# Kernel optimization log

Measured on AMD Instinct MI355X. Metric: run time of the kernel, lower is better.

Reference implementation:

```python
import math
import jax, jax.numpy as jnp
import numpy as np

R, N, B, E, H, M = 128, 256, 1, 512, 8, 4
D = E // H
NEG = -1e9  # eye-mask fill value from masked_fill(-1000000000)


def setup_inputs() -> dict:
    key = jax.random.key(0)
    ks = jax.random.split(key, 10)
    p = lambda k, shape: jax.random.normal(k, shape, jnp.float32) * 0.02
    z = lambda n: jnp.zeros((n,), jnp.float32)
    return {
        "x": jax.random.normal(ks[0], (R, N, B, E), jnp.float32),
        "network": jax.random.uniform(ks[1], (B, N, N, M), jnp.float32),
        "Wq": p(ks[2], (E, E)), "bq": z(E),
        "Wk": p(ks[3], (E, E)), "bk": z(E),
        "Wv": p(ks[4], (E, E)), "bv": z(E),
        "Wo": p(ks[5], (E, E)), "bo": z(E),
        "Wq1": p(ks[6], (D, 8)), "bq1": z(8),
        "Wk1": p(ks[7], (1, 8)), "bk1": z(8),
        "l": jax.random.normal(ks[8], (H, 1, 1, 1), jnp.float32),
    }


def reference(x, network, Wq, bq, Wk, bk, Wv, bv, Wo, bo, Wq1, bq1, Wk1, bk1, l):
    # x: [R, N, B, E]; network: [B, N, N, M] (B must be 1, as in the torch module)
    scaling = (D ** -0.5) / math.sqrt(R)  # align_scaling

    q = (x @ Wq + bq).reshape(R, N, B, H, D) * scaling
    k = (x @ Wk + bk).reshape(R, N, B, H, D)

    # shared contraction: summed over rows r, kept per head-dim d -> [H, B, N, N, D]
    qk = jnp.einsum('rinhd,rjnhd->hnijd', q, k)

    # network-bias MLP branch
    q1 = (qk @ Wq1 + bq1).mean(0)                  # [B, N, N, 8]
    network_k = network[..., None] * Wk1[0] + bk1  # Linear(1,8): [B, N, N, M, 8]
    net_attn = jnp.einsum('nijd,nijmd->nijm', q1, network_k)  # [B, N, N, M]
    net_attn = jnp.tile(net_attn, (H, 1, 1, 1))    # repeat over heads (B==1) -> [H, N, N, M]

    # attn_weights 'rinhd,rjnhd->hnij' == qk summed over d
    attn_weights = qk.sum(-1)                      # [H, B, N, N]

    net_probs = jax.nn.softmax(net_attn, axis=-1)  # softmax over M network channels
    net_bias = (network * net_probs).sum(-1)[:, None, :, :]  # [H, 1(B), N, N]
    attn_weights = attn_weights + l * net_bias

    eye = jnp.eye(N, dtype=bool)
    attn_weights = jnp.where(eye, NEG, attn_weights)
    attn_probs = jax.nn.softmax(attn_weights, axis=-1)  # [H, B, N, N]

    v = (x @ Wv + bv).reshape(R, N, B, H, D)
    context = jnp.einsum('hnij,rjnhd->rinhd', attn_probs, v).reshape(R, N, B, E)
    output = context @ Wo + bo
    return (output, attn_probs, l)
```

## Files before the change

kernel.cpp:

```cpp
#include <hip/hip_runtime.h>
#include <hip/hip_bf16.h>
#include <cmath>
#include <stdint.h>

using bf16 = __hip_bfloat16;
typedef __attribute__((ext_vector_type(8))) short bf16x8;
typedef __attribute__((ext_vector_type(4))) float f32x4;

constexpr int LDT  = 40;
constexpr int LDTB = 34;

__device__ __forceinline__ void gload16(const bf16* g, bf16* l)
{
  __builtin_amdgcn_global_load_lds(
      (const __attribute__((address_space(1))) void*)g,
      (__attribute__((address_space(3))) void*)l,
      16, 0, 0);
}

__global__ __launch_bounds__(256)
void k_convert_x(const float* __restrict__ x, bf16* __restrict__ xb)
{
  const long idx = (long)blockIdx.x * 256 + threadIdx.x;
  const float4 f0 = *(const float4*)&x[idx * 8];
  const float4 f1 = *(const float4*)&x[idx * 8 + 4];
  alignas(16) bf16 t[8] = {
    __float2bfloat16(f0.x), __float2bfloat16(f0.y),
    __float2bfloat16(f0.z), __float2bfloat16(f0.w),
    __float2bfloat16(f1.x), __float2bfloat16(f1.y),
    __float2bfloat16(f1.z), __float2bfloat16(f1.w)};
  *(uint4*)&xb[idx * 8] = *(const uint4*)t;
}

__global__ __launch_bounds__(256)
void k_prep_w(const float* __restrict__ Wq, const float* __restrict__ Wk,
              const float* __restrict__ Wv, const float* __restrict__ Wo,
              bf16* __restrict__ WT, float scaling)
{
  const int sel = blockIdx.z;
  const float* W = sel == 0 ? Wq : sel == 1 ? Wk : sel == 2 ? Wv : Wo;
  const float sc = sel == 0 ? scaling : 1.0f;
  const int k0 = blockIdx.x * 64, n0 = blockIdx.y * 64;
  __shared__ float tile[64][68];
  const int tid = threadIdx.x;
  #pragma unroll
  for (int it = 0; it < 4; it++) {
    const int c = tid + it * 256;
    const int kk = c >> 4, nn4 = (c & 15) * 4;
    const float4 v = *(const float4*)&W[(long)(k0 + kk) * 512 + n0 + nn4];
    tile[kk][nn4] = v.x; tile[kk][nn4 + 1] = v.y;
    tile[kk][nn4 + 2] = v.z; tile[kk][nn4 + 3] = v.w;
  }
  __syncthreads();
  #pragma unroll
  for (int it = 0; it < 2; it++) {
    const int c = tid + it * 256;
    const int nn = c >> 3, k8 = (c & 7) * 8;
    alignas(16) bf16 t[8];
    #pragma unroll
    for (int jj = 0; jj < 8; jj++) t[jj] = __float2bfloat16(tile[k8 + jj][nn] * sc);
    *(uint4*)&WT[(long)(sel * 512 + n0 + nn) * 512 + k0 + k8] = *(const uint4*)t;
  }
}

__global__ void k_prep_small(const float* __restrict__ bq, const float* __restrict__ bk,
                             const float* __restrict__ bv, const float* __restrict__ bo,
                             const float* __restrict__ Wq1, const float* __restrict__ Wk1,
                             float* __restrict__ bias_all, float* __restrict__ u, float scaling)
{
  const int idx = blockIdx.x * 256 + threadIdx.x;
  const int s2 = idx >> 9, n2 = idx & 511;
  const float* b = s2 == 0 ? bq : s2 == 1 ? bk : s2 == 2 ? bv : bo;
  bias_all[idx] = b[n2] * (s2 == 0 ? scaling : 1.0f);
  if (idx < 64) {
    float s = 0.0f;
    #pragma unroll
    for (int c = 0; c < 8; c++) s += Wq1[idx * 8 + c] * Wk1[c];
    u[idx] = s;
  }
}

__global__ __launch_bounds__(256)
void gemm_qkv(const bf16* __restrict__ xb, const bf16* __restrict__ WT,
              const float* __restrict__ bias_all,
              bf16* __restrict__ Qn, bf16* __restrict__ Kn, bf16* __restrict__ Vn)
{
  __shared__ bf16 As[2][128 * 32];
  __shared__ bf16 Bs[2][128 * 32];
  const int tid = threadIdx.x, lane = tid & 63;
  const int wid = tid >> 6, wr = wid >> 1, wc = wid & 1;
  const int lr = lane & 15, lk = (lane >> 4) * 8;
  const int flat = (blockIdx.x & 7) * 384 + (blockIdx.x >> 3);
  const int m0 = (flat / 12) * 128, n0 = (flat % 12) * 128;
  const int c1 = tid + 256;
  const int ra0 = tid >> 2, pa0 = (tid & 3) * 8;
  const int ra1 = c1 >> 2,  pa1 = (c1 & 3) * 8;
  f32x4 acc[4][4] = {};

  auto stage = [&](int b, int k0) {
    gload16(&xb[(long)(m0 + ra0) * 512 + k0 + pa0], &As[b][tid * 8]);
    gload16(&xb[(long)(m0 + ra1) * 512 + k0 + pa1], &As[b][c1 * 8]);
    gload16(&WT[(long)(n0 + ra0) * 512 + k0 + pa0], &Bs[b][tid * 8]);
    gload16(&WT[(long)(n0 + ra1) * 512 + k0 + pa1], &Bs[b][c1 * 8]);
  };

  stage(0, 0);
  asm volatile("s_waitcnt vmcnt(0)" ::: "memory");
  __syncthreads();

  int buf = 0;
  for (int t = 0; t < 16; ++t) {
    if (t < 15) stage(buf ^ 1, (t + 1) * 32);
    bf16x8 af[4], bfr[4];
    #pragma unroll
    for (int m = 0; m < 4; m++)
      af[m] = *(const bf16x8*)&As[buf][(wr * 64 + m * 16 + lr) * 32 + lk];
    #pragma unroll
    for (int n = 0; n < 4; n++)
      bfr[n] = *(const bf16x8*)&Bs[buf][(wc * 64 + n * 16 + lr) * 32 + lk];
    #pragma unroll
    for (int m = 0; m < 4; m++)
      #pragma unroll
      for (int n = 0; n < 4; n++)
        acc[m][n] = __builtin_amdgcn_mfma_f32_16x16x32_bf16(af[m], bfr[n], acc[m][n], 0, 0, 0);
    asm volatile("s_waitcnt vmcnt(0)" ::: "memory");
    __syncthreads();
    buf ^= 1;
  }

  const int er = (lane >> 4) * 4, ec = lane & 15;
  #pragma unroll
  for (int m = 0; m < 4; m++) {
    const int row0 = m0 + wr * 64 + m * 16 + er;
    #pragma unroll
    for (int n = 0; n < 4; n++) {
      const int col = n0 + wc * 64 + n * 16 + ec;
      const float bv = bias_all[col];
      #pragma unroll
      for (int q = 0; q < 4; q++) {
        const float v = acc[m][n][q] + bv;
        const long row = row0 + q;
        if (col < 512)       Qn[row * 512 + col]        = __float2bfloat16(v);
        else if (col < 1024) Kn[row * 512 + col - 512]  = __float2bfloat16(v);
        else                 Vn[row * 512 + col - 1024] = __float2bfloat16(v);
      }
    }
  }
}

__global__ __launch_bounds__(256)
void gemm_logits(const bf16* __restrict__ Qn, const bf16* __restrict__ Kn,
                 const float* __restrict__ u, float* __restrict__ part)
{
  __shared__ bf16 As[2][128 * 32];
  __shared__ bf16 Bs[2][128 * 32];
  __shared__ float us[64];
  const int tid = threadIdx.x, lane = tid & 63;
  const int wid = tid >> 6, wr = wid >> 1, wc = wid & 1;
  const int lr = lane & 15, lk = (lane >> 4) * 8;
  const int z = blockIdx.z, batch = z >> 3, ks = z & 7, h = batch & 7;
  const bool uscale = batch >= 8;
  const int m0 = blockIdx.y * 128, n0 = blockIdx.x * 128;
  if (tid < 64) us[tid] = u[tid];
  __syncthreads();
  const int c1 = tid + 256;
  const int ra0 = tid >> 2, pa0 = (tid & 3) * 8;
  const int ra1 = c1 >> 2,  pa1 = (c1 & 3) * 8;
  f32x4 acc[4][4] = {};

  auto gk_of = [&](int kk) { return ks * 1024 + kk * 32; };

  {
    const int gk = gk_of(0), r = gk >> 6, d0 = gk & 63;
    const long ab = (long)(r * 256 + m0) * 512 + h * 64 + d0;
    const long bb = (long)(r * 256 + n0) * 512 + h * 64 + d0;
    gload16(&Kn[bb + (long)ra0 * 512 + pa0], &Bs[0][tid * 8]);
    gload16(&Kn[bb + (long)ra1 * 512 + pa1], &Bs[0][c1 * 8]);
    if (!uscale) {
      gload16(&Qn[ab + (long)ra0 * 512 + pa0], &As[0][tid * 8]);
      gload16(&Qn[ab + (long)ra1 * 512 + pa1], &As[0][c1 * 8]);
    } else {
      const uint4 v0 = *(const uint4*)&Qn[ab + (long)ra0 * 512 + pa0];
      const uint4 v1 = *(const uint4*)&Qn[ab + (long)ra1 * 512 + pa1];
      const unsigned short* p0 = (const unsigned short*)&v0;
      const unsigned short* p1 = (const unsigned short*)&v1;
      alignas(16) bf16 t0[8], t1[8];
      #pragma unroll
      for (int jj = 0; jj < 8; jj++) {
        t0[jj] = __float2bfloat16(__bfloat162float(*(const bf16*)&p0[jj]) * us[d0 + pa0 + jj]);
        t1[jj] = __float2bfloat16(__bfloat162float(*(const bf16*)&p1[jj]) * us[d0 + pa1 + jj]);
      }
      *(uint4*)&As[0][tid * 8] = *(const uint4*)t0;
      *(uint4*)&As[0][c1 * 8] = *(const uint4*)t1;
    }
  }
  __syncthreads();

  int buf = 0;
  for (int kk = 0; kk < 32; ++kk) {
    uint4 va0, va1;
    int d0n = 0;
    if (kk < 31) {
      const int gk = gk_of(kk + 1), r = gk >> 6;
      d0n = gk & 63;
      const long ab = (long)(r * 256 + m0) * 512 + h * 64 + d0n;
      const long bb = (long)(r * 256 + n0) * 512 + h * 64 + d0n;
      gload16(&Kn[bb + (long)ra0 * 512 + pa0], &Bs[buf ^ 1][tid * 8]);
      gload16(&Kn[bb + (long)ra1 * 512 + pa1], &Bs[buf ^ 1][c1 * 8]);
      if (!uscale) {
        gload16(&Qn[ab + (long)ra0 * 512 + pa0], &As[buf ^ 1][tid * 8]);
        gload16(&Qn[ab + (long)ra1 * 512 + pa1], &As[buf ^ 1][c1 * 8]);
      } else {
        va0 = *(const uint4*)&Qn[ab + (long)ra0 * 512 + pa0];
        va1 = *(const uint4*)&Qn[ab + (long)ra1 * 512 + pa1];
      }
    }
    bf16x8 af[4], bfr[4];
    #pragma unroll
    for (int m = 0; m < 4; m++)
      af[m] = *(const bf16x8*)&As[buf][(wr * 64 + m * 16 + lr) * 32 + lk];
    #pragma unroll
    for (int n = 0; n < 4; n++)
      bfr[n] = *(const bf16x8*)&Bs[buf][(wc * 64 + n * 16 + lr) * 32 + lk];
    #pragma unroll
    for (int m = 0; m < 4; m++)
      #pragma unroll
      for (int n = 0; n < 4; n++)
        acc[m][n] = __builtin_amdgcn_mfma_f32_16x16x32_bf16(af[m], bfr[n], acc[m][n], 0, 0, 0);
    if (uscale && kk < 31) {
      const unsigned short* p0 = (const unsigned short*)&va0;
      const unsigned short* p1 = (const unsigned short*)&va1;
      alignas(16) bf16 t0[8], t1[8];
      #pragma unroll
      for (int jj = 0; jj < 8; jj++) {
        t0[jj] = __float2bfloat16(__bfloat162float(*(const bf16*)&p0[jj]) * us[d0n + pa0 + jj]);
        t1[jj] = __float2bfloat16(__bfloat162float(*(const bf16*)&p1[jj]) * us[d0n + pa1 + jj]);
      }
      *(uint4*)&As[buf ^ 1][tid * 8] = *(const uint4*)t0;
      *(uint4*)&As[buf ^ 1][c1 * 8] = *(const uint4*)t1;
    }
    __syncthreads();
    buf ^= 1;
  }

  float* C = part + (long)z * 65536;
  const int er = (lane >> 4) * 4, ec = lane & 15;
  #pragma unroll
  for (int m = 0; m < 4; m++)
    #pragma unroll
    for (int n = 0; n < 4; n++) {
      const int col = n0 + wc * 64 + n * 16 + ec;
      #pragma unroll
      for (int q = 0; q < 4; q++)
        C[(long)(m0 + wr * 64 + m * 16 + er + q) * 256 + col] = acc[m][n][q];
    }
}

__global__ __launch_bounds__(128)
void gemm_ctx(const bf16* __restrict__ Pb, const bf16* __restrict__ Vn,
              bf16* __restrict__ ctxb)
{
  __shared__ bf16 As[128 * LDT];
  __shared__ bf16 Bs[64 * LDTB];
  const int m0 = blockIdx.x * 128, r = blockIdx.y, h = blockIdx.z;
  const int tid = threadIdx.x, lane = tid & 63, wid = tid >> 6;
  const int wr = wid;
  const int lr = lane & 15, lk = (lane >> 4) * 8;
  const bf16* A = Pb + (long)h * 65536;
  f32x4 acc[4][4] = {};

  for (int j0 = 0; j0 < 256; j0 += 32) {
    #pragma unroll
    for (int c = tid; c < 512; c += 128) {
      const int row = c >> 2, k8 = (c & 3) * 8;
      *(uint4*)&As[row * LDT + k8] = *(const uint4*)&A[(long)(m0 + row) * 256 + j0 + k8];
    }
    #pragma unroll
    for (int c = tid; c < 256; c += 128) {
      const int jj = c >> 3, d8 = (c & 7) * 8;
      const uint4 v = *(const uint4*)&Vn[((long)(r * 256 + j0 + jj)) * 512 + h * 64 + d8];
      const unsigned short* pv = (const unsigned short*)&v;
      #pragma unroll
      for (int t = 0; t < 8; t++)
        *(unsigned short*)&Bs[(d8 + t) * LDTB + jj] = pv[t];
    }
    __syncthreads();
    bf16x8 af[4], bfr[4];
    #pragma unroll
    for (int m = 0; m < 4; m++)
      af[m] = *(const bf16x8*)&As[(wr * 64 + m * 16 + lr) * LDT + lk];
    #pragma unroll
    for (int n = 0; n < 4; n++)
      bfr[n] = *(const bf16x8*)&Bs[(n * 16 + lr) * LDTB + lk];
    #pragma unroll
    for (int m = 0; m < 4; m++)
      #pragma unroll
      for (int n = 0; n < 4; n++)
        acc[m][n] = __builtin_amdgcn_mfma_f32_16x16x32_bf16(af[m], bfr[n], acc[m][n], 0, 0, 0);
    __syncthreads();
  }

  const int er = (lane >> 4) * 4, ec = lane & 15;
  #pragma unroll
  for (int m = 0; m < 4; m++) {
    const int i0 = m0 + wr * 64 + m * 16 + er;
    #pragma unroll
    for (int n = 0; n < 4; n++) {
      const int d = n * 16 + ec;
      #pragma unroll
      for (int q = 0; q < 4; q++)
        ctxb[((long)(r * 256 + i0 + q)) * 512 + h * 64 + d] = __float2bfloat16(acc[m][n][q]);
    }
  }
}

__global__ __launch_bounds__(512)
void gemm_outp(const bf16* __restrict__ A, const bf16* __restrict__ B,
               float* __restrict__ C, const float* __restrict__ bias)
{
  __shared__ bf16 As[2][128 * 32];
  __shared__ bf16 Bs[2][256 * 32];
  const int tid = threadIdx.x, lane = tid & 63, wid = tid >> 6;
  const int wr = wid >> 2, wc = wid & 3;
  const int lr = lane & 15, lk = (lane >> 4) * 8;
  const int m0 = blockIdx.y * 128, n0 = blockIdx.x * 256;
  const int ra = tid >> 2, pa = (tid & 3) * 8;
  const int cb1 = tid + 512;
  const int rb0 = tid >> 2, pb0 = (tid & 3) * 8;
  const int rb1 = cb1 >> 2, pb1 = (cb1 & 3) * 8;
  f32x4 acc[4][4] = {};

  gload16(&A[(long)(m0 + ra) * 512 + pa], &As[0][tid * 8]);
  gload16(&B[(long)(n0 + rb0) * 512 + pb0], &Bs[0][tid * 8]);
  gload16(&B[(long)(n0 + rb1) * 512 + pb1], &Bs[0][cb1 * 8]);
  __syncthreads();

  int buf = 0;
  for (int t = 0; t < 16; ++t) {
    const int k0n = (t + 1) * 32;
    if (t < 15) {
      gload16(&A[(long)(m0 + ra) * 512 + k0n + pa], &As[buf ^ 1][tid * 8]);
      gload16(&B[(long)(n0 + rb0) * 512 + k0n + pb0], &Bs[buf ^ 1][tid * 8]);
      gload16(&B[(long)(n0 + rb1) * 512 + k0n + pb1], &Bs[buf ^ 1][cb1 * 8]);
    }
    bf16x8 af[4], bfr[4];
    #pragma unroll
    for (int m = 0; m < 4; m++)
      af[m] = *(const bf16x8*)&As[buf][(wr * 64 + m * 16 + lr) * 32 + lk];
    #pragma unroll
    for (int n = 0; n < 4; n++)
      bfr[n] = *(const bf16x8*)&Bs[buf][(wc * 64 + n * 16 + lr) * 32 + lk];
    #pragma unroll
    for (int m = 0; m < 4; m++)
      #pragma unroll
      for (int n = 0; n < 4; n++)
        acc[m][n] = __builtin_amdgcn_mfma_f32_16x16x32_bf16(af[m], bfr[n], acc[m][n], 0, 0, 0);
    __syncthreads();
    buf ^= 1;
  }

  const int er = (lane >> 4) * 4, ec = lane & 15;
  #pragma unroll
  for (int m = 0; m < 4; m++) {
    const int row0 = m0 + wr * 64 + m * 16 + er;
    #pragma unroll
    for (int n = 0; n < 4; n++) {
      const int col = n0 + wc * 64 + n * 16 + ec;
      const float bv = bias[col];
      #pragma unroll
      for (int q = 0; q < 4; q++)
        C[(long)(row0 + q) * 512 + col] = acc[m][n][q] + bv;
    }
  }
}

__global__ void k_bias(const float* __restrict__ part, const float* __restrict__ network,
                       const float* __restrict__ bq1, const float* __restrict__ Wk1,
                       float* __restrict__ net_bias)
{
  const int i = blockIdx.x, j = threadIdx.x;
  float c1 = 0.0f;
  #pragma unroll
  for (int c = 0; c < 8; c++) c1 += bq1[c] * Wk1[c];
  float s1 = 0.0f;
  const long ij = i * 256 + j;
  #pragma unroll
  for (int s = 64; s < 128; s++) s1 += part[(long)s * 65536 + ij];
  s1 = 0.125f * s1 + c1;
  const float4 nw = *(const float4*)&network[ij * 4];
  const float a0 = nw.x * s1, a1 = nw.y * s1, a2 = nw.z * s1, a3 = nw.w * s1;
  const float mx = fmaxf(fmaxf(a0, a1), fmaxf(a2, a3));
  const float e0 = expf(a0 - mx), e1 = expf(a1 - mx), e2 = expf(a2 - mx), e3 = expf(a3 - mx);
  const float inv = 1.0f / (e0 + e1 + e2 + e3);
  net_bias[ij] = (nw.x * e0 + nw.y * e1 + nw.z * e2 + nw.w * e3) * inv;
}

__global__ void k_softmax(const float* __restrict__ part, const float* __restrict__ net_bias,
                          const float* __restrict__ l, float* __restrict__ out_probs,
                          bf16* __restrict__ Pb, float* __restrict__ out_l)
{
  const int i = blockIdx.x, h = blockIdx.y, j = threadIdx.x;
  const long ij = i * 256 + j;
  float w = 0.0f;
  #pragma unroll
  for (int ks = 0; ks < 8; ks++) w += part[(long)(h * 8 + ks) * 65536 + ij];
  w += l[h] * net_bias[ij];
  if (j == i) w = -1e9f;
  float m = w;
  #pragma unroll
  for (int o = 32; o; o >>= 1) m = fmaxf(m, __shfl_xor(m, o));
  __shared__ float red[4], red2[4];
  if ((j & 63) == 0) red[j >> 6] = m;
  __syncthreads();
  m = fmaxf(fmaxf(red[0], red[1]), fmaxf(red[2], red[3]));
  const float e = expf(w - m);
  float s = e;
  #pragma unroll
  for (int o = 32; o; o >>= 1) s += __shfl_xor(s, o);
  if ((j & 63) == 0) red2[j >> 6] = s;
  __syncthreads();
  s = red2[0] + red2[1] + red2[2] + red2[3];
  const float p = e / s;
  out_probs[(long)h * 65536 + ij] = p;
  Pb[(long)h * 65536 + ij] = __float2bfloat16(p);
  if (h == 0 && i == 0 && j < 8) out_l[j] = l[j];
}

extern "C" void kernel_launch(void* const* d_in, const int* in_sizes, int n_in,
                              void* d_out, int out_size, void* d_ws, size_t ws_size,
                              hipStream_t stream)
{
  const float* x   = (const float*)d_in[0];
  const float* net = (const float*)d_in[1];
  const float* Wq  = (const float*)d_in[2];
  const float* bq  = (const float*)d_in[3];
  const float* Wk  = (const float*)d_in[4];
  const float* bk  = (const float*)d_in[5];
  const float* Wv  = (const float*)d_in[6];
  const float* bv  = (const float*)d_in[7];
  const float* Wo  = (const float*)d_in[8];
  const float* bo  = (const float*)d_in[9];
  const float* Wq1 = (const float*)d_in[10];
  const float* bq1 = (const float*)d_in[11];
  const float* Wk1 = (const float*)d_in[12];
  const float* l   = (const float*)d_in[14];
  float* out = (float*)d_out;

  bf16* Qn = (bf16*)d_out;
  bf16* Kn = Qn + 16777216;

  char* ws = (char*)d_ws;
  size_t off = 0;
  auto alloc = [&](size_t bytes) { char* p = ws + off; off += (bytes + 255) & ~255ULL; return p; };
  bf16*  WT       = (bf16*)alloc(2048ULL * 512 * 2);
  float* bias_all = (float*)alloc(2048 * 4);
  float* u        = (float*)alloc(64 * 4);
  bf16*  xb       = (bf16*)alloc(16777216ULL * 2);
  bf16*  Vn       = (bf16*)alloc(16777216ULL * 2);
  float* net_bias = (float*)alloc(65536ULL * 4);
  bf16*  Pb       = (bf16*)alloc(8ULL * 65536 * 2);
  float* part     = (float*)xb;
  bf16*  ctxb     = xb;

  const float scaling = (float)(0.125 / sqrt(128.0));

  k_convert_x<<<8192, 256, 0, stream>>>(x, xb);
  k_prep_w<<<dim3(8, 8, 4), 256, 0, stream>>>(Wq, Wk, Wv, Wo, WT, scaling);
  k_prep_small<<<8, 256, 0, stream>>>(bq, bk, bv, bo, Wq1, Wk1, bias_all, u, scaling);

  gemm_qkv<<<3072, 256, 0, stream>>>(xb, WT, bias_all, Qn, Kn, Vn);

  gemm_logits<<<dim3(2, 2, 128), 256, 0, stream>>>(Qn, Kn, u, part);

  k_bias<<<256, 256, 0, stream>>>(part, net, bq1, Wk1, net_bias);
  k_softmax<<<dim3(256, 8, 1), 256, 0, stream>>>(part, net_bias, l,
                                                 out + 16777216, Pb, out + 17301504);

  gemm_ctx<<<dim3(2, 128, 8), 128, 0, stream>>>(Pb, Vn, ctxb);

  gemm_outp<<<dim3(2, 256, 1), 512, 0, stream>>>(ctxb, WT + 1536 * 512, out, bias_all + 1536);
}
```

Baseline: 219.1 us.

## XOR-swizzle LDS tiles in GEMMs and triple-buffer the QKV projection

Applies an XOR swizzle to the k-chunk position of each 16-byte LDS store and to the matching fragment read offset in the QKV, logits and output-projection GEMMs, to cut LDS bank conflicts on the MFMA operand reads. The QKV GEMM also moves from double to triple buffering with partial vmcnt waits, so loads run two stages ahead and the wait before the second barrier is gone. This uses more LDS per block, which may lower occupancy, and the swizzle must stay consistent between global source addresses and LDS reads.

```diff
diff --git a/kernel.cpp b/kernel.cpp
--- a/kernel.cpp
+++ b/kernel.cpp
@@ -17,6 +17,8 @@
       (__attribute__((address_space(3))) void*)l,
       16, 0, 0);
 }
+
+__device__ __forceinline__ int swsrc(int c) { return (((c & 3) ^ ((c >> 3) & 3)) * 8); }
 
 __global__ __launch_bounds__(256)
 void k_convert_x(const float* __restrict__ x, bf16* __restrict__ xb)
@@ -85,47 +87,49 @@
               const float* __restrict__ bias_all,
               bf16* __restrict__ Qn, bf16* __restrict__ Kn, bf16* __restrict__ Vn)
 {
-  __shared__ bf16 As[2][128 * 32];
-  __shared__ bf16 Bs[2][128 * 32];
+  __shared__ bf16 As[3][128 * 32];
+  __shared__ bf16 Bs[3][128 * 32];
   const int tid = threadIdx.x, lane = tid & 63;
   const int wid = tid >> 6, wr = wid >> 1, wc = wid & 1;
-  const int lr = lane & 15, lk = (lane >> 4) * 8;
+  const int lr = lane & 15;
+  const int lkx = ((lane >> 4) ^ ((lane >> 1) & 3)) * 8;
   const int flat = (blockIdx.x & 7) * 384 + (blockIdx.x >> 3);
   const int m0 = (flat / 12) * 128, n0 = (flat % 12) * 128;
   const int c1 = tid + 256;
-  const int ra0 = tid >> 2, pa0 = (tid & 3) * 8;
-  const int ra1 = c1 >> 2,  pa1 = (c1 & 3) * 8;
+  const int ra0 = tid >> 2, ra1 = c1 >> 2;
+  const int ps = swsrc(tid);
   f32x4 acc[4][4] = {};
 
   auto stage = [&](int b, int k0) {
-    gload16(&xb[(long)(m0 + ra0) * 512 + k0 + pa0], &As[b][tid * 8]);
-    gload16(&xb[(long)(m0 + ra1) * 512 + k0 + pa1], &As[b][c1 * 8]);
-    gload16(&WT[(long)(n0 + ra0) * 512 + k0 + pa0], &Bs[b][tid * 8]);
-    gload16(&WT[(long)(n0 + ra1) * 512 + k0 + pa1], &Bs[b][c1 * 8]);
+    gload16(&xb[(long)(m0 + ra0) * 512 + k0 + ps], &As[b][tid * 8]);
+    gload16(&xb[(long)(m0 + ra1) * 512 + k0 + ps], &As[b][c1 * 8]);
+    gload16(&WT[(long)(n0 + ra0) * 512 + k0 + ps], &Bs[b][tid * 8]);
+    gload16(&WT[(long)(n0 + ra1) * 512 + k0 + ps], &Bs[b][c1 * 8]);
   };
 
   stage(0, 0);
-  asm volatile("s_waitcnt vmcnt(0)" ::: "memory");
-  __syncthreads();
-
-  int buf = 0;
+  stage(1, 32);
+
   for (int t = 0; t < 16; ++t) {
-    if (t < 15) stage(buf ^ 1, (t + 1) * 32);
+    const int cur = t % 3;
+    if (t < 14) stage((t + 2) % 3, (t + 2) * 32);
+    if (t < 14)      asm volatile("s_waitcnt vmcnt(8)" ::: "memory");
+    else if (t < 15) asm volatile("s_waitcnt vmcnt(4)" ::: "memory");
+    else             asm volatile("s_waitcnt vmcnt(0)" ::: "memory");
+    __syncthreads();
     bf16x8 af[4], bfr[4];
     #pragma unroll
     for (int m = 0; m < 4; m++)
-      af[m] = *(const bf16x8*)&As[buf][(wr * 64 + m * 16 + lr) * 32 + lk];
+      af[m] = *(const bf16x8*)&As[cur][(wr * 64 + m * 16 + lr) * 32 + lkx];
     #pragma unroll
     for (int n = 0; n < 4; n++)
-      bfr[n] = *(const bf16x8*)&Bs[buf][(wc * 64 + n * 16 + lr) * 32 + lk];
+      bfr[n] = *(const bf16x8*)&Bs[cur][(wc * 64 + n * 16 + lr) * 32 + lkx];
     #pragma unroll
     for (int m = 0; m < 4; m++)
       #pragma unroll
       for (int n = 0; n < 4; n++)
         acc[m][n] = __builtin_amdgcn_mfma_f32_16x16x32_bf16(af[m], bfr[n], acc[m][n], 0, 0, 0);
-    asm volatile("s_waitcnt vmcnt(0)" ::: "memory");
-    __syncthreads();
-    buf ^= 1;
+    __syncthreads();
   }
 
   const int er = (lane >> 4) * 4, ec = lane & 15;
@@ -157,15 +161,16 @@
   __shared__ float us[64];
   const int tid = threadIdx.x, lane = tid & 63;
   const int wid = tid >> 6, wr = wid >> 1, wc = wid & 1;
-  const int lr = lane & 15, lk = (lane >> 4) * 8;
+  const int lr = lane & 15;
+  const int lkx = ((lane >> 4) ^ ((lane >> 1) & 3)) * 8;
   const int z = blockIdx.z, batch = z >> 3, ks = z & 7, h = batch & 7;
   const bool uscale = batch >= 8;
   const int m0 = blockIdx.y * 128, n0 = blockIdx.x * 128;
   if (tid < 64) us[tid] = u[tid];
   __syncthreads();
   const int c1 = tid + 256;
-  const int ra0 = tid >> 2, pa0 = (tid & 3) * 8;
-  const int ra1 = c1 >> 2,  pa1 = (c1 & 3) * 8;
+  const int ra0 = tid >> 2, ra1 = c1 >> 2;
+  const int ps = swsrc(tid);
   f32x4 acc[4][4] = {};
 
   auto gk_of = [&](int kk) { return ks * 1024 + kk * 32; };
@@ -174,21 +179,21 @@
     const int gk = gk_of(0), r = gk >> 6, d0 = gk & 63;
     const long ab = (long)(r * 256 + m0) * 512 + h * 64 + d0;
     const long bb = (long)(r * 256 + n0) * 512 + h * 64 + d0;
-    gload16(&Kn[bb + (long)ra0 * 512 + pa0], &Bs[0][tid * 8]);
-    gload16(&Kn[bb + (long)ra1 * 512 + pa1], &Bs[0][c1 * 8]);
+    gload16(&Kn[bb + (long)ra0 * 512 + ps], &Bs[0][tid * 8]);
+    gload16(&Kn[bb + (long)ra1 * 512 + ps], &Bs[0][c1 * 8]);
     if (!uscale) {
-      gload16(&Qn[ab + (long)ra0 * 512 + pa0], &As[0][tid * 8]);
-      gload16(&Qn[ab + (long)ra1 * 512 + pa1], &As[0][c1 * 8]);
+      gload16(&Qn[ab + (long)ra0 * 512 + ps], &As[0][tid * 8]);
+      gload16(&Qn[ab + (long)ra1 * 512 + ps], &As[0][c1 * 8]);
     } else {
-      const uint4 v0 = *(const uint4*)&Qn[ab + (long)ra0 * 512 + pa0];
-      const uint4 v1 = *(const uint4*)&Qn[ab + (long)ra1 * 512 + pa1];
+      const uint4 v0 = *(const uint4*)&Qn[ab + (long)ra0 * 512 + ps];
+      const uint4 v1 = *(const uint4*)&Qn[ab + (long)ra1 * 512 + ps];
       const unsigned short* p0 = (const unsigned short*)&v0;
       const unsigned short* p1 = (const unsigned short*)&v1;
       alignas(16) bf16 t0[8], t1[8];
       #pragma unroll
       for (int jj = 0; jj < 8; jj++) {
-        t0[jj] = __float2bfloat16(__bfloat162float(*(const bf16*)&p0[jj]) * us[d0 + pa0 + jj]);
-        t1[jj] = __float2bfloat16(__bfloat162float(*(const bf16*)&p1[jj]) * us[d0 + pa1 + jj]);
+        t0[jj] = __float2bfloat16(__bfloat162float(*(const bf16*)&p0[jj]) * us[d0 + ps + jj]);
+        t1[jj] = __float2bfloat16(__bfloat162float(*(const bf16*)&p1[jj]) * us[d0 + ps + jj]);
       }
       *(uint4*)&As[0][tid * 8] = *(const uint4*)t0;
       *(uint4*)&As[0][c1 * 8] = *(const uint4*)t1;
@@ -205,23 +210,23 @@
       d0n = gk & 63;
       const long ab = (long)(r * 256 + m0) * 512 + h * 64 + d0n;
       const long bb = (long)(r * 256 + n0) * 512 + h * 64 + d0n;
-      gload16(&Kn[bb + (long)ra0 * 512 + pa0], &Bs[buf ^ 1][tid * 8]);
-      gload16(&Kn[bb + (long)ra1 * 512 + pa1], &Bs[buf ^ 1][c1 * 8]);
+      gload16(&Kn[bb + (long)ra0 * 512 + ps], &Bs[buf ^ 1][tid * 8]);
+      gload16(&Kn[bb + (long)ra1 * 512 + ps], &Bs[buf ^ 1][c1 * 8]);
       if (!uscale) {
-        gload16(&Qn[ab + (long)ra0 * 512 + pa0], &As[buf ^ 1][tid * 8]);
-        gload16(&Qn[ab + (long)ra1 * 512 + pa1], &As[buf ^ 1][c1 * 8]);
+        gload16(&Qn[ab + (long)ra0 * 512 + ps], &As[buf ^ 1][tid * 8]);
+        gload16(&Qn[ab + (long)ra1 * 512 + ps], &As[buf ^ 1][c1 * 8]);
       } else {
-        va0 = *(const uint4*)&Qn[ab + (long)ra0 * 512 + pa0];
-        va1 = *(const uint4*)&Qn[ab + (long)ra1 * 512 + pa1];
+        va0 = *(const uint4*)&Qn[ab + (long)ra0 * 512 + ps];
+        va1 = *(const uint4*)&Qn[ab + (long)ra1 * 512 + ps];
       }
     }
     bf16x8 af[4], bfr[4];
     #pragma unroll
     for (int m = 0; m < 4; m++)
-      af[m] = *(const bf16x8*)&As[buf][(wr * 64 + m * 16 + lr) * 32 + lk];
+      af[m] = *(const bf16x8*)&As[buf][(wr * 64 + m * 16 + lr) * 32 + lkx];
     #pragma unroll
     for (int n = 0; n < 4; n++)
-      bfr[n] = *(const bf16x8*)&Bs[buf][(wc * 64 + n * 16 + lr) * 32 + lk];
+      bfr[n] = *(const bf16x8*)&Bs[buf][(wc * 64 + n * 16 + lr) * 32 + lkx];
     #pragma unroll
     for (int m = 0; m < 4; m++)
       #pragma unroll
@@ -233,8 +238,8 @@
       alignas(16) bf16 t0[8], t1[8];
       #pragma unroll
       for (int jj = 0; jj < 8; jj++) {
-        t0[jj] = __float2bfloat16(__bfloat162float(*(const bf16*)&p0[jj]) * us[d0n + pa0 + jj]);
-        t1[jj] = __float2bfloat16(__bfloat162float(*(const bf16*)&p1[jj]) * us[d0n + pa1 + jj]);
+        t0[jj] = __float2bfloat16(__bfloat162float(*(const bf16*)&p0[jj]) * us[d0n + ps + jj]);
+        t1[jj] = __float2bfloat16(__bfloat162float(*(const bf16*)&p1[jj]) * us[d0n + ps + jj]);
       }
       *(uint4*)&As[buf ^ 1][tid * 8] = *(const uint4*)t0;
       *(uint4*)&As[buf ^ 1][c1 * 8] = *(const uint4*)t1;
@@ -322,34 +327,35 @@
   __shared__ bf16 Bs[2][256 * 32];
   const int tid = threadIdx.x, lane = tid & 63, wid = tid >> 6;
   const int wr = wid >> 2, wc = wid & 3;
-  const int lr = lane & 15, lk = (lane >> 4) * 8;
+  const int lr = lane & 15;
+  const int lkx = ((lane >> 4) ^ ((lane >> 1) & 3)) * 8;
   const int m0 = blockIdx.y * 128, n0 = blockIdx.x * 256;
-  const int ra = tid >> 2, pa = (tid & 3) * 8;
+  const int ra = tid >> 2;
   const int cb1 = tid + 512;
-  const int rb0 = tid >> 2, pb0 = (tid & 3) * 8;
-  const int rb1 = cb1 >> 2, pb1 = (cb1 & 3) * 8;
+  const int rb0 = tid >> 2, rb1 = cb1 >> 2;
+  const int ps = swsrc(tid);
   f32x4 acc[4][4] = {};
 
-  gload16(&A[(long)(m0 + ra) * 512 + pa], &As[0][tid * 8]);
-  gload16(&B[(long)(n0 + rb0) * 512 + pb0], &Bs[0][tid * 8]);
-  gload16(&B[(long)(n0 + rb1) * 512 + pb1], &Bs[0][cb1 * 8]);
+  gload16(&A[(long)(m0 + ra) * 512 + ps], &As[0][tid * 8]);
+  gload16(&B[(long)(n0 + rb0) * 512 + ps], &Bs[0][tid * 8]);
+  gload16(&B[(long)(n0 + rb1) * 512 + ps], &Bs[0][cb1 * 8]);
   __syncthreads();
 
   int buf = 0;
   for (int t = 0; t < 16; ++t) {
     const int k0n = (t + 1) * 32;
     if (t < 15) {
-      gload16(&A[(long)(m0 + ra) * 512 + k0n + pa], &As[buf ^ 1][tid * 8]);
-      gload16(&B[(long)(n0 + rb0) * 512 + k0n + pb0], &Bs[buf ^ 1][tid * 8]);
-      gload16(&B[(long)(n0 + rb1) * 512 + k0n + pb1], &Bs[buf ^ 1][cb1 * 8]);
+      gload16(&A[(long)(m0 + ra) * 512 + k0n + ps], &As[buf ^ 1][tid * 8]);
+      gload16(&B[(long)(n0 + rb0) * 512 + k0n + ps], &Bs[buf ^ 1][tid * 8]);
+      gload16(&B[(long)(n0 + rb1) * 512 + k0n + ps], &Bs[buf ^ 1][cb1 * 8]);
     }
     bf16x8 af[4], bfr[4];
     #pragma unroll
     for (int m = 0; m < 4; m++)
-      af[m] = *(const bf16x8*)&As[buf][(wr * 64 + m * 16 + lr) * 32 + lk];
+      af[m] = *(const bf16x8*)&As[buf][(wr * 64 + m * 16 + lr) * 32 + lkx];
     #pragma unroll
     for (int n = 0; n < 4; n++)
-      bfr[n] = *(const bf16x8*)&Bs[buf][(wc * 64 + n * 16 + lr) * 32 + lk];
+      bfr[n] = *(const bf16x8*)&Bs[buf][(wc * 64 + n * 16 + lr) * 32 + lkx];
     #pragma unroll
     for (int m = 0; m < 4; m++)
       #pragma unroll
```

Measured after the change: 213.4 us. 1.03x faster.
